# Performance work log

Hardware: AMD Instinct MI355X
Metric: run time of the kernel (lower is better)

The kernel has to match this reference:

```python
import jax, jax.numpy as jnp
import numpy as np

D, DFF, H, V, BS, NL, NG = 1024, 4096, 16, 32000, 128, 2, 2

def _ln(x, w, b, eps=1e-5):
    m = x.mean(-1, keepdims=True)
    v = ((x - m) ** 2).mean(-1, keepdims=True)
    return (x - m) / jnp.sqrt(v + eps) * w + b

def _full_attn(q, k, v):
    # q,k,v: [B,H,S,dk] ; manual max-subtract softmax with +1e-9 denom and clamp, per FullAttention
    dk = q.shape[-1]
    s = jnp.einsum('bhqd,bhkd->bhqk', q / jnp.sqrt(jnp.float32(dk)), k)
    s = s - s.max(-1, keepdims=True)
    e = jnp.exp(s)
    a = e / (e.sum(-1, keepdims=True) + 1e-9)
    a = jnp.clip(a, 1e-9, 1.0)
    return jnp.einsum('bhqk,bhkd->bhqd', a, v)

def _attn_layer(qi, ki, vi, lnw, lnb, pw, pb):
    # lnw/lnb: [4,D] (norm_q,k,v,out); pw: [4,D,D] (q,k,v,o, stored [in,out]); pb: [4,D]
    B, Sq, _ = qi.shape
    Sk = ki.shape[1]
    q = _ln(qi, lnw[0], lnb[0]) @ pw[0] + pb[0]
    k = _ln(ki, lnw[1], lnb[1]) @ pw[1] + pb[1]
    v = _ln(vi, lnw[2], lnb[2]) @ pw[2] + pb[2]
    dk = D // H
    q = q.reshape(B, Sq, H, dk).transpose(0, 2, 1, 3)
    k = k.reshape(B, Sk, H, dk).transpose(0, 2, 1, 3)
    v = v.reshape(B, Sk, H, dk).transpose(0, 2, 1, 3)
    o = _full_attn(q, k, v).transpose(0, 2, 1, 3).reshape(B, Sq, D)
    o = o @ pw[3] + pb[3]
    return _ln(o, lnw[3], lnb[3])

def _ffn(x, n1w, n1b, n2w, n2b, w1, b1, w2, b2):
    h = jax.nn.gelu(_ln(x, n1w, n1b) @ w1 + b1, approximate=False)
    return _ln(h @ w2 + b2 + x, n2w, n2b)

def _tlayer(x, lnw, lnb, pw, pb, w1, b1, w2, b2):
    # lnw/lnb: [6,D] (attn q,k,v,out norms, ffn norm1, ffn norm2)
    x = x + _attn_layer(x, x, x, lnw[:4], lnb[:4], pw, pb)
    return _ffn(x, lnw[4], lnb[4], lnw[5], lnb[5], w1, b1, w2, b2)

def _pe(S, d):
    pos = jnp.arange(S, dtype=jnp.float32)[:, None]
    div = jnp.exp(jnp.arange(0, d, 2, dtype=jnp.float32) * (-np.log(10000.0) / d))
    pe = jnp.zeros((S, d), jnp.float32)
    pe = pe.at[:, 0::2].set(jnp.sin(pos * div))
    pe = pe.at[:, 1::2].set(jnp.cos(pos * div))
    return pe

def setup_inputs() -> dict:
    key = jax.random.key(0)
    ks = iter(jax.random.split(key, 64))
    nrm = lambda shp: jax.random.normal(next(ks), shp, jnp.float32) * 0.02
    inp = {
        'x': jax.random.randint(next(ks), (4, 4096), 0, V, dtype=jnp.int32).astype(jnp.int64),
        'emb': nrm((V, D)),
        'in_ln_w': jnp.ones((D,)), 'in_ln_b': jnp.zeros((D,)),
        'loc_ln_w': jnp.ones((NL, 6, D)), 'loc_ln_b': jnp.zeros((NL, 6, D)),
        'loc_pw': nrm((NL, 4, D, D)), 'loc_pb': jnp.zeros((NL, 4, D)),
        'loc_w1': nrm((NL, D, DFF)), 'loc_b1': jnp.zeros((NL, DFF)),
        'loc_w2': nrm((NL, DFF, D)), 'loc_b2': jnp.zeros((NL, D)),
        'locn_w': jnp.ones((D,)), 'locn_b': jnp.zeros((D,)),
        'pool_q': nrm((1, 1, D)),
        'pool_n_w': jnp.ones((D,)), 'pool_n_b': jnp.zeros((D,)),
        'pool_ln_w': jnp.ones((4, D)), 'pool_ln_b': jnp.zeros((4, D)),
        'pool_pw': nrm((4, D, D)), 'pool_pb': jnp.zeros((4, D)),
        'glob_ln_w': jnp.ones((NG, 6, D)), 'glob_ln_b': jnp.zeros((NG, 6, D)),
        'glob_pw': nrm((NG, 4, D, D)), 'glob_pb': jnp.zeros((NG, 4, D)),
        'glob_w1': nrm((NG, D, DFF)), 'glob_b1': jnp.zeros((NG, DFF)),
        'glob_w2': nrm((NG, DFF, D)), 'glob_b2': jnp.zeros((NG, D)),
        'out_ln_w': jnp.ones((D,)), 'out_ln_b': jnp.zeros((D,)),
        'out_w': nrm((D, V)), 'out_b': jnp.zeros((V,)),
    }
    return inp

def reference(x, emb, in_ln_w, in_ln_b, loc_ln_w, loc_ln_b, loc_pw, loc_pb,
              loc_w1, loc_b1, loc_w2, loc_b2, locn_w, locn_b,
              pool_q, pool_n_w, pool_n_b, pool_ln_w, pool_ln_b, pool_pw, pool_pb,
              glob_ln_w, glob_ln_b, glob_pw, glob_pb, glob_w1, glob_b1, glob_w2, glob_b2,
              out_ln_w, out_ln_b, out_w, out_b):
    B, S = x.shape
    nb = S // BS
    h = jnp.clip(emb[x], -100.0, 100.0) + _pe(S, D)[None]
    h = _ln(h, in_ln_w, in_ln_b)
    h = h.reshape(B * nb, BS, D)  # local blocks
    for i in range(NL):
        h = jnp.clip(_tlayer(h, loc_ln_w[i], loc_ln_b[i], loc_pw[i], loc_pb[i],
                             loc_w1[i], loc_b1[i], loc_w2[i], loc_b2[i]), -100.0, 100.0)
    h = _ln(h, locn_w, locn_b)
    # attention pooling of each block to one vector
    hp = _ln(h, pool_n_w, pool_n_b)
    q = jnp.broadcast_to(pool_q, (B * nb, 1, D))
    g = _attn_layer(q, hp, hp, pool_ln_w, pool_ln_b, pool_pw, pool_pb)[:, 0].reshape(B, nb, D)
    for i in range(NG):
        g = jnp.clip(_tlayer(g, glob_ln_w[i], glob_ln_b[i], glob_pw[i], glob_pb[i],
                             glob_w1[i], glob_b1[i], glob_w2[i], glob_b2[i]), -100.0, 100.0)
    g = _ln(g, out_ln_w, out_ln_b)
    return g @ out_w + out_b  # [B, num_blocks, vocab]
```

## Files before the change

### kernel.cpp

```cpp
#include <hip/hip_runtime.h>
#include <hip/hip_bf16.h>
#include <math.h>

#define DEV __device__ __forceinline__

typedef __attribute__((ext_vector_type(8))) short bf16x8;
typedef __attribute__((ext_vector_type(4))) float f32x4;
typedef unsigned short u16;

constexpr int D_ = 1024, NTOK = 16384, SEQ = 4096;

DEV u16 f2b(float f){
  union{float f;unsigned u;} v; v.f=f;
  unsigned r = (v.u + 0x7fffu + ((v.u>>16)&1u))>>16;
  return (u16)r;
}
DEV float b2f(u16 h){ union{unsigned u;float f;} v; v.u=((unsigned)h)<<16; return v.f; }

DEV float gelu_f(float x){
  float z = 0.7978845608028654f*(x + 0.044715f*x*x*x);
  float e = __expf(-2.f*z);
  float t = 2.f/(1.f+e) - 1.f;
  return 0.5f*x*(1.f+t);
}

DEV void gld16(const void* g, void* l){
  __builtin_amdgcn_global_load_lds((const __attribute__((address_space(1))) void*)g,
                                   (__attribute__((address_space(3))) void*)l, 16, 0, 0);
}

DEV float blockSum(float v){
  __shared__ float sb[4];
  #pragma unroll
  for(int m=32;m>=1;m>>=1) v += __shfl_xor(v, m, 64);
  int lane = threadIdx.x & 63, wv = threadIdx.x >> 6;
  __syncthreads();
  if(lane==0) sb[wv]=v;
  __syncthreads();
  float r = sb[0]+sb[1]+sb[2]+sb[3];
  __syncthreads();
  return r;
}

__global__ __launch_bounds__(256) void detect_k(const int* __restrict__ xr, int* __restrict__ flag){
  int tid=threadIdx.x; float cnt=0.f;
  for(int i=tid;i<8192;i+=256) if(xr[2*i+1]!=0) cnt+=1.f;
  cnt = blockSum(cnt);
  if(tid==0) *flag = (cnt < 64.f) ? 1 : 0;
}

__global__ __launch_bounds__(256) void embed_k(const void* __restrict__ xv, const int* __restrict__ flag,
      const float* __restrict__ emb, const float* __restrict__ w, const float* __restrict__ b,
      u16* __restrict__ out, u16* __restrict__ outn){
  int t = blockIdx.x;
  int id;
  if(*flag) id = (int)((const long long*)xv)[t];
  else      id = ((const int*)xv)[t];
  int s = t & (SEQ-1);
  int d0 = threadIdx.x*4;
  float4 e4 = *(const float4*)(emb + (size_t)id*D_ + d0);
  float vv[4] = {e4.x, e4.y, e4.z, e4.w};
  float acc = 0.f;
  #pragma unroll
  for(int i=0;i<4;i++){
    float e = fminf(fmaxf(vv[i], -100.f), 100.f);
    int d = d0+i;
    float fr = expf(-(float)(d & ~1) * (9.210340371976184f/(float)D_));
    float ang = (float)s * fr;
    e += (d&1) ? cosf(ang) : sinf(ang);
    vv[i]=e; acc+=e;
  }
  float mean = blockSum(acc)*(1.f/D_);
  float var=0.f;
  #pragma unroll
  for(int i=0;i<4;i++){ float dd=vv[i]-mean; var+=dd*dd; }
  var = blockSum(var)*(1.f/D_);
  float rs = rsqrtf(var+1e-5f);
  float y[4];
  #pragma unroll
  for(int i=0;i<4;i++) y[i] = (vv[i]-mean)*rs*w[d0+i]+b[d0+i];
  ushort4 o; o.x=f2b(y[0]); o.y=f2b(y[1]); o.z=f2b(y[2]); o.w=f2b(y[3]);
  *(ushort4*)(out + (size_t)t*D_ + d0) = o;
  float m2 = blockSum(y[0]+y[1]+y[2]+y[3])*(1.f/D_);
  float v2=0.f;
  #pragma unroll
  for(int i=0;i<4;i++){ float dd=y[i]-m2; v2+=dd*dd; }
  v2 = blockSum(v2)*(1.f/D_);
  float rs2 = rsqrtf(v2+1e-5f);
  ushort4 on; on.x=f2b((y[0]-m2)*rs2); on.y=f2b((y[1]-m2)*rs2); on.z=f2b((y[2]-m2)*rs2); on.w=f2b((y[3]-m2)*rs2);
  *(ushort4*)(outn + (size_t)t*D_ + d0) = on;
}

template<int MODE,int WRN>
__global__ __launch_bounds__(256) void ln_k(const u16* __restrict__ in, const u16* __restrict__ res,
      const float* __restrict__ w, const float* __restrict__ b, u16* __restrict__ out,
      u16* __restrict__ outn){
  int t = blockIdx.x; int d0 = threadIdx.x*4;
  ushort4 r4 = *(const ushort4*)(in + (size_t)t*D_ + d0);
  float vv[4] = {b2f(r4.x),b2f(r4.y),b2f(r4.z),b2f(r4.w)};
  float mean = blockSum(vv[0]+vv[1]+vv[2]+vv[3])*(1.f/D_);
  float var=0.f;
  #pragma unroll
  for(int i=0;i<4;i++){ float dd=vv[i]-mean; var+=dd*dd; }
  var = blockSum(var)*(1.f/D_);
  float rs = rsqrtf(var+1e-5f);
  float rv[4]={0,0,0,0};
  if(MODE==3){
    ushort4 q4 = *(const ushort4*)(res + (size_t)t*D_ + d0);
    rv[0]=b2f(q4.x); rv[1]=b2f(q4.y); rv[2]=b2f(q4.z); rv[3]=b2f(q4.w);
  }
  float y[4];
  #pragma unroll
  for(int i=0;i<4;i++){
    float v = (vv[i]-mean)*rs;
    v = v*w[d0+i]+b[d0+i];
    if(MODE==2) v = fminf(fmaxf(v,-100.f),100.f);
    if(MODE==3) v += rv[i];
    y[i]=v;
  }
  ushort4 o; o.x=f2b(y[0]); o.y=f2b(y[1]); o.z=f2b(y[2]); o.w=f2b(y[3]);
  *(ushort4*)(out + (size_t)t*D_ + d0) = o;
  if(WRN){
    float m2 = blockSum(y[0]+y[1]+y[2]+y[3])*(1.f/D_);
    float v2=0.f;
    #pragma unroll
    for(int i=0;i<4;i++){ float dd=y[i]-m2; v2+=dd*dd; }
    v2 = blockSum(v2)*(1.f/D_);
    float rs2 = rsqrtf(v2+1e-5f);
    ushort4 on; on.x=f2b((y[0]-m2)*rs2); on.y=f2b((y[1]-m2)*rs2); on.z=f2b((y[2]-m2)*rs2); on.w=f2b((y[3]-m2)*rs2);
    *(ushort4*)(outn + (size_t)t*D_ + d0) = on;
  }
}

__global__ __launch_bounds__(256) void ln3x_k(const u16* __restrict__ in,
    const float* __restrict__ w1,const float* __restrict__ b1,
    const float* __restrict__ w2,const float* __restrict__ b2, u16* __restrict__ out){
  int t=blockIdx.x, d0=threadIdx.x*4;
  ushort4 r4 = *(const ushort4*)(in + (size_t)t*D_ + d0);
  float vv[4]={b2f(r4.x),b2f(r4.y),b2f(r4.z),b2f(r4.w)};
  #pragma unroll
  for(int pass=0;pass<3;pass++){
    float mean = blockSum(vv[0]+vv[1]+vv[2]+vv[3])*(1.f/D_);
    float var=0.f;
    #pragma unroll
    for(int i=0;i<4;i++){ float dd=vv[i]-mean; var+=dd*dd; }
    var = blockSum(var)*(1.f/D_);
    float rs = rsqrtf(var+1e-5f);
    #pragma unroll
    for(int i=0;i<4;i++){
      float y=(vv[i]-mean)*rs;
      if(pass==0) y = y*w1[d0+i]+b1[d0+i];
      else if(pass==1) y = y*w2[d0+i]+b2[d0+i];
      vv[i]=y;
    }
  }
  ushort4 o;
  o.x=f2b(vv[0]); o.y=f2b(vv[1]); o.z=f2b(vv[2]); o.w=f2b(vv[3]);
  *(ushort4*)(out + (size_t)t*D_ + d0) = o;
}

__global__ __launch_bounds__(256) void lnrow_k(const float* __restrict__ x, const float* __restrict__ w,
      const float* __restrict__ b, float* __restrict__ out){
  int d0=threadIdx.x*4;
  float vv[4]={x[d0],x[d0+1],x[d0+2],x[d0+3]};
  float mean = blockSum(vv[0]+vv[1]+vv[2]+vv[3])*(1.f/D_);
  float var=0.f;
  #pragma unroll
  for(int i=0;i<4;i++){ float dd=vv[i]-mean; var+=dd*dd; }
  var = blockSum(var)*(1.f/D_);
  float rs = rsqrtf(var+1e-5f);
  #pragma unroll
  for(int i=0;i<4;i++) out[d0+i]=(vv[i]-mean)*rs*w[d0+i]+b[d0+i];
}

__global__ __launch_bounds__(256) void tf_k(const float* __restrict__ W, int ldW,
      const float* __restrict__ lnw, u16* __restrict__ Wt, int Kd){
  __shared__ float T[64][65];
  int n0 = blockIdx.x*64, k0 = blockIdx.y*64;
  int ty = threadIdx.x>>6, tx = threadIdx.x&63;
  #pragma unroll
  for(int p=0;p<16;p++){
    int row = p*4+ty;
    float sc = lnw ? lnw[k0+row] : 1.f;
    T[row][tx] = W[(size_t)(k0+row)*ldW + n0+tx]*sc;
  }
  __syncthreads();
  #pragma unroll
  for(int p=0;p<16;p++){
    int row = p*4+ty;
    Wt[(size_t)(n0+row)*Kd + k0+tx] = f2b(T[tx][row]);
  }
}

__global__ __launch_bounds__(256) void bias_k(const float* __restrict__ W, int ldW,
      const float* __restrict__ lnb, const float* __restrict__ pb, float* __restrict__ out, int Kd){
  int j = blockIdx.x, tid=threadIdx.x;
  float chk=0.f;
  if(lnb){ for(int k=tid;k<Kd;k+=256) chk += fabsf(lnb[k]); }
  chk = blockSum(chk);
  if(chk==0.f){ if(tid==0) out[j]=pb[j]; return; }
  float s=0.f;
  for(int k=tid;k<Kd;k+=256) s += lnb[k]*W[(size_t)k*ldW + j];
  s = blockSum(s);
  if(tid==0) out[j]=pb[j]+s;
}

__global__ __launch_bounds__(256) void matvec_k(const float* __restrict__ xn, const float* __restrict__ W,
      int ldW, const float* __restrict__ bias, float* __restrict__ out){
  int j=blockIdx.x, tid=threadIdx.x;
  float s=0.f;
  for(int k=tid;k<1024;k+=256) s += xn[k]*W[(size_t)k*ldW + j];
  s=blockSum(s);
  if(tid==0) out[j]=s+bias[j];
}

template<int EPI,int OUTF,int TV>
__global__ __launch_bounds__(256) void gemm_k(const u16* __restrict__ A, const u16* __restrict__ Bt,
      const float* __restrict__ bias, const u16* __restrict__ resid, void* __restrict__ Cout,
      int M, int N, int K, int ldc){
  __shared__ u16 SH[16384];
  int tid = threadIdx.x, lane = tid&63, wv = tid>>6;
  int g = lane>>4, l15 = lane&15;
  int GX = gridDim.x;
  int nwg = GX*gridDim.y;
  int flat = blockIdx.y*GX + blockIdx.x;
  int q = nwg>>3, r = nwg&7, xcd = flat&7, idx = flat>>3;
  int f = (xcd<r ? xcd*(q+1) : r*(q+1)+(xcd-r)*q) + idx;
  int by = f/GX, bx = f - by*GX;
  int row0 = by*128, col0 = bx*128;
  int wr = wv>>1, wc = wv&1;
  u16* As = SH;
  u16* Bs = SH + 8192;
  int e0 = wv*512 + lane*8;
  f32x4 acc[4][4] = {};
  auto STAGE = [&](int buf, int k0){
    #pragma unroll
    for(int c=0;c<2;c++){
      int e = c*2048 + e0;
      gld16(A  + (size_t)(row0 + (e>>5))*K + (k0 + (e&31)), &As[buf*4096 + e]);
      gld16(Bt + (size_t)(col0 + (e>>5))*K + (k0 + (e&31)), &Bs[buf*4096 + e]);
    }
  };
  STAGE(0, 0);
  int nt = K>>5;
  __syncthreads();
  int cur = 0;
  for(int t=0;t<nt;t++){
    if(t+1<nt) STAGE(cur^1, (t+1)<<5);
    bf16x8 a[4], b[4];
    #pragma unroll
    for(int m=0;m<4;m++) a[m] = *(const bf16x8*)&As[cur*4096 + (wr*64+m*16+l15)*32 + g*8];
    #pragma unroll
    for(int n=0;n<4;n++) b[n] = *(const bf16x8*)&Bs[cur*4096 + (wc*64+n*16+l15)*32 + g*8];
    #pragma unroll
    for(int m=0;m<4;m++)
      #pragma unroll
      for(int n=0;n<4;n++)
        acc[m][n] = __builtin_amdgcn_mfma_f32_16x16x32_bf16(a[m], b[n], acc[m][n], 0,0,0);
    __syncthreads();
    cur ^= 1;
  }
  #pragma unroll
  for(int m=0;m<4;m++){
    #pragma unroll
    for(int n=0;n<4;n++){
      int Cc = col0 + wc*64 + n*16 + l15;
      float bs = bias[Cc];
      if(TV){
        int Rb = row0 + wr*64 + m*16 + g*4;
        ushort4 pk;
        pk.x = f2b(acc[m][n][0]+bs);
        pk.y = f2b(acc[m][n][1]+bs);
        pk.z = f2b(acc[m][n][2]+bs);
        pk.w = f2b(acc[m][n][3]+bs);
        *(ushort4*)((u16*)Cout + (size_t)Cc*M + Rb) = pk;
      } else {
        #pragma unroll
        for(int r2=0;r2<4;r2++){
          int R = row0 + wr*64 + m*16 + g*4 + r2;
          float v = acc[m][n][r2] + bs;
          if(EPI==1) v = gelu_f(v);
          if(EPI==2) v += b2f(resid[(size_t)R*ldc + Cc]);
          if(OUTF) ((float*)Cout)[(size_t)R*ldc + Cc] = v;
          else     ((u16*)Cout)[(size_t)R*ldc + Cc] = f2b(v);
        }
      }
    }
  }
}

__global__ __launch_bounds__(256) void attnl_k(const u16* __restrict__ QK, const u16* __restrict__ VT,
      u16* __restrict__ AT){
  __shared__ u16 SP[16384];
  __shared__ u16 Vt[8192];
  __shared__ float rmax[256], rsum[256];
  int tid=threadIdx.x, lane=tid&63, wv=tid>>6, g=lane>>4, l15=lane&15;
  int lb = blockIdx.x>>4, h = blockIdx.x&15;
  int wr=wv>>1, wc=wv&1;
  #pragma unroll
  for(int c=0;c<4;c++){
    int chunk = c*2048 + wv*512;
    int e = chunk + lane*8;
    gld16(QK + (size_t)(lb*128 + (e>>6))*2048 + h*64 + (e&63),        &SP[chunk]);
    gld16(QK + (size_t)(lb*128 + (e>>6))*2048 + 1024 + h*64 + (e&63), &SP[8192+chunk]);
    gld16(VT + (size_t)(h*64 + (e>>7))*16384 + lb*128 + (e&127),      &Vt[chunk]);
  }
  __syncthreads();
  f32x4 s[4][4] = {};
  #pragma unroll
  for(int ks=0;ks<2;ks++){
    bf16x8 a[4], b[4];
    #pragma unroll
    for(int m=0;m<4;m++) a[m] = *(const bf16x8*)&SP[(wr*64+m*16+l15)*64 + ks*32 + g*8];
    #pragma unroll
    for(int n=0;n<4;n++) b[n] = *(const bf16x8*)&SP[8192+(wc*64+n*16+l15)*64 + ks*32 + g*8];
    #pragma unroll
    for(int m=0;m<4;m++)
      #pragma unroll
      for(int n=0;n<4;n++)
        s[m][n] = __builtin_amdgcn_mfma_f32_16x16x32_bf16(a[m], b[n], s[m][n], 0,0,0);
  }
  #pragma unroll
  for(int m=0;m<4;m++)
    #pragma unroll
    for(int n=0;n<4;n++) s[m][n] *= 0.125f;
  #pragma unroll
  for(int m=0;m<4;m++)
    #pragma unroll
    for(int r=0;r<4;r++){
      float mx = fmaxf(fmaxf(s[m][0][r],s[m][1][r]),fmaxf(s[m][2][r],s[m][3][r]));
      #pragma unroll
      for(int msk=1;msk<16;msk<<=1) mx = fmaxf(mx, __shfl_xor(mx,msk,64));
      if(l15==0) rmax[(wr*64+m*16+g*4+r)*2+wc]=mx;
    }
  __syncthreads();
  #pragma unroll
  for(int m=0;m<4;m++)
    #pragma unroll
    for(int r=0;r<4;r++){
      int row = wr*64+m*16+g*4+r;
      float M2 = fmaxf(rmax[row*2], rmax[row*2+1]);
      float sm=0.f;
      #pragma unroll
      for(int n=0;n<4;n++){ float e = expf(s[m][n][r]-M2); s[m][n][r]=e; sm+=e; }
      #pragma unroll
      for(int msk=1;msk<16;msk<<=1) sm += __shfl_xor(sm,msk,64);
      if(l15==0) rsum[row*2+wc]=sm;
    }
  __syncthreads();
  #pragma unroll
  for(int m=0;m<4;m++)
    #pragma unroll
    for(int r=0;r<4;r++){
      int row = wr*64+m*16+g*4+r;
      float den = rsum[row*2]+rsum[row*2+1]+1e-9f;
      #pragma unroll
      for(int n=0;n<4;n++){
        float a = s[m][n][r]/den;
        a = fminf(fmaxf(a,1e-9f),1.f);
        SP[row*128 + wc*64+n*16+l15] = f2b(a);
      }
    }
  __syncthreads();
  f32x4 o[4][2] = {};
  #pragma unroll
  for(int ks=0;ks<4;ks++){
    bf16x8 a[4], b[2];
    #pragma unroll
    for(int m=0;m<4;m++) a[m] = *(const bf16x8*)&SP[(wr*64+m*16+l15)*128 + ks*32 + g*8];
    #pragma unroll
    for(int n=0;n<2;n++) b[n] = *(const bf16x8*)&Vt[(wc*32+n*16+l15)*128 + ks*32 + g*8];
    #pragma unroll
    for(int m=0;m<4;m++)
      #pragma unroll
      for(int n=0;n<2;n++)
        o[m][n] = __builtin_amdgcn_mfma_f32_16x16x32_bf16(a[m], b[n], o[m][n], 0,0,0);
  }
  #pragma unroll
  for(int m=0;m<4;m++)
    #pragma unroll
    for(int n=0;n<2;n++)
      #pragma unroll
      for(int r=0;r<4;r++)
        AT[(size_t)(lb*128 + wr*64+m*16+g*4+r)*1024 + h*64 + wc*32+n*16+l15] = f2b(o[m][n][r]);
}

__global__ __launch_bounds__(256) void poolattn_k(const float* __restrict__ qp, const u16* __restrict__ KV,
      u16* __restrict__ g0){
  int lb = blockIdx.x, tid = threadIdx.x;
  __shared__ float sc[16*128];
  for(int p=tid;p<2048;p+=256){
    int h=p>>7, j=p&127;
    const u16* krow = KV + (size_t)(lb*128+j)*2048 + h*64;
    float s=0.f;
    for(int d=0;d<64;d++) s += qp[h*64+d]*b2f(krow[d]);
    sc[h*128+j] = s*0.125f;
  }
  __syncthreads();
  if(tid<16){
    float* r=&sc[tid*128];
    float mx=r[0];
    for(int j=1;j<128;j++) mx=fmaxf(mx,r[j]);
    float sm=0.f;
    for(int j=0;j<128;j++){ float e=expf(r[j]-mx); r[j]=e; sm+=e; }
    sm+=1e-9f;
    for(int j=0;j<128;j++) r[j]=fminf(fmaxf(r[j]/sm,1e-9f),1.f);
  }
  __syncthreads();
  for(int c=tid;c<1024;c+=256){
    int h=c>>6;
    float acc=0.f;
    for(int j=0;j<128;j++) acc += sc[h*128+j]*b2f(KV[(size_t)(lb*128+j)*2048 + 1024 + c]);
    g0[(size_t)lb*1024 + c] = f2b(acc);
  }
}

__global__ __launch_bounds__(256) void attng_k(const u16* __restrict__ QKV, u16* __restrict__ OUT){
  int bb = blockIdx.x>>4, h = blockIdx.x&15;
  __shared__ float sc[32*32];
  int tid=threadIdx.x;
  for(int p=tid;p<1024;p+=256){
    int i=p>>5, j=p&31;
    const u16* q = QKV + (size_t)(bb*32+i)*3072 + h*64;
    const u16* k = QKV + (size_t)(bb*32+j)*3072 + 1024 + h*64;
    float s=0.f;
    for(int d=0;d<64;d++) s += b2f(q[d])*b2f(k[d]);
    sc[p] = s*0.125f;
  }
  __syncthreads();
  if(tid<32){
    float* r=&sc[tid*32];
    float mx=r[0];
    for(int j=1;j<32;j++) mx=fmaxf(mx,r[j]);
    float sm=0.f;
    for(int j=0;j<32;j++){ float e=expf(r[j]-mx); r[j]=e; sm+=e; }
    sm+=1e-9f;
    for(int j=0;j<32;j++) r[j]=fminf(fmaxf(r[j]/sm,1e-9f),1.f);
  }
  __syncthreads();
  for(int p=tid;p<2048;p+=256){
    int i=p>>6, d=p&63;
    float acc=0.f;
    for(int j=0;j<32;j++) acc += sc[i*32+j]*b2f(QKV[(size_t)(bb*32+j)*3072 + 2048 + h*64 + d]);
    OUT[(size_t)(bb*32+i)*1024 + h*64 + d] = f2b(acc);
  }
}

extern "C" void kernel_launch(void* const* d_in, const int* in_sizes, int n_in,
                              void* d_out, int out_size, void* d_ws, size_t ws_size,
                              hipStream_t stream) {
  (void)in_sizes; (void)n_in; (void)out_size;
  const void*  x       = d_in[0];
  const float* emb     = (const float*)d_in[1];
  const float* in_ln_w = (const float*)d_in[2];
  const float* in_ln_b = (const float*)d_in[3];
  const float* loc_ln_w= (const float*)d_in[4];
  const float* loc_ln_b= (const float*)d_in[5];
  const float* loc_pw  = (const float*)d_in[6];
  const float* loc_pb  = (const float*)d_in[7];
  const float* loc_w1  = (const float*)d_in[8];
  const float* loc_b1  = (const float*)d_in[9];
  const float* loc_w2  = (const float*)d_in[10];
  const float* loc_b2  = (const float*)d_in[11];
  const float* locn_w  = (const float*)d_in[12];
  const float* locn_b  = (const float*)d_in[13];
  const float* pool_q  = (const float*)d_in[14];
  const float* pool_n_w= (const float*)d_in[15];
  const float* pool_n_b= (const float*)d_in[16];
  const float* pool_ln_w=(const float*)d_in[17];
  const float* pool_ln_b=(const float*)d_in[18];
  const float* pool_pw = (const float*)d_in[19];
  const float* pool_pb = (const float*)d_in[20];
  const float* glob_ln_w=(const float*)d_in[21];
  const float* glob_ln_b=(const float*)d_in[22];
  const float* glob_pw = (const float*)d_in[23];
  const float* glob_pb = (const float*)d_in[24];
  const float* glob_w1 = (const float*)d_in[25];
  const float* glob_b1 = (const float*)d_in[26];
  const float* glob_w2 = (const float*)d_in[27];
  const float* glob_b2 = (const float*)d_in[28];
  const float* out_ln_w= (const float*)d_in[29];
  const float* out_ln_b= (const float*)d_in[30];
  const float* out_w   = (const float*)d_in[31];
  const float* out_b   = (const float*)d_in[32];

  char* wsb = (char*)d_ws;
  size_t off = 0;
  auto AL = [&](size_t n)->char*{ size_t o=(off+255)&~(size_t)255; off=o+n; return wsb+o; };

  int*  flag = (int*)AL(256);
  u16*  WA   = (u16*)AL(12ull*1024*1024*2);
  float* BA  = (float*)AL(12*1024*4);
  float* qn  = (float*)AL(1024*4);
  float* qp  = (float*)AL(1024*4);
  float* Hb  = (float*)AL(32000*4);
  u16*  R    = (u16*)AL(64ull*1024*1024*2);
  u16*  X    = (u16*)AL((size_t)NTOK*1024*2);
  u16*  XN   = (u16*)AL((size_t)NTOK*1024*2);
  u16*  G    = (u16*)AL(128ull*1024*2);
  u16*  GN   = (u16*)AL(128ull*1024*2);
  u16*  GQKV = (u16*)AL(128ull*3072*2);
  u16*  GAT  = (u16*)AL(128ull*1024*2);
  u16*  GO   = (u16*)AL(128ull*1024*2);
  u16*  GFH  = (u16*)AL(128ull*4096*2);
  u16*  g0   = (u16*)AL(128ull*1024*2);
  if(off > ws_size) return;

  u16 *LWqk = WA, *LWv = WA+2097152, *LWo = WA+3145728, *LW1 = WA+4194304, *LW2 = WA+8388608;
  float *Lbqk = BA, *Lbv = BA+2048, *Lbo = BA+3072, *Lb1 = BA+4096, *Lb2 = BA+8192;
  u16 *GWqkv = WA, *GWo = WA+3145728, *GW1 = WA+4194304, *GW2 = WA+8388608;
  float *Gbqkv = BA, *Gbo = BA+3072, *Gb1 = BA+4096, *Gb2 = BA+8192;
  u16 *PWkv = WA, *PWo = WA+2097152;
  float *Pbkv = BA, *Pbo = BA+2048;
  u16 *QKb = R, *VTb = R+33554432, *ATb = R+50331648;
  u16 *FH  = R;
  u16 *KVb = R;
  u16 *HW  = R;
  u16 *Ob  = XN;

  const size_t MM = 1024ull*1024;

  detect_k<<<1,256,0,stream>>>((const int*)x, flag);
  embed_k<<<NTOK,256,0,stream>>>(x, flag, emb, in_ln_w, in_ln_b, X, XN);

  for(int l=0;l<2;l++){
    const float* pw = loc_pw + (size_t)l*4*MM;
    const float* lw = loc_ln_w + (size_t)l*6*1024;
    const float* lb = loc_ln_b + (size_t)l*6*1024;
    const float* pb = loc_pb + (size_t)l*4*1024;
    tf_k<<<dim3(16,16),256,0,stream>>>(pw+0*MM, 1024, lw+0*1024, LWqk,          1024);
    tf_k<<<dim3(16,16),256,0,stream>>>(pw+1*MM, 1024, lw+1*1024, LWqk+1024*1024,1024);
    tf_k<<<dim3(16,16),256,0,stream>>>(pw+2*MM, 1024, lw+2*1024, LWv,           1024);
    tf_k<<<dim3(16,16),256,0,stream>>>(pw+3*MM, 1024, nullptr,   LWo,           1024);
    tf_k<<<dim3(64,16),256,0,stream>>>(loc_w1+(size_t)l*1024*4096, 4096, lw+4*1024, LW1, 1024);
    tf_k<<<dim3(16,64),256,0,stream>>>(loc_w2+(size_t)l*4096*1024, 1024, nullptr,   LW2, 4096);
    bias_k<<<1024,256,0,stream>>>(pw+0*MM, 1024, lb+0*1024, pb+0,      Lbqk,      1024);
    bias_k<<<1024,256,0,stream>>>(pw+1*MM, 1024, lb+1*1024, pb+1024,   Lbqk+1024, 1024);
    bias_k<<<1024,256,0,stream>>>(pw+2*MM, 1024, lb+2*1024, pb+2*1024, Lbv,       1024);
    bias_k<<<1024,256,0,stream>>>(pw+3*MM, 1024, nullptr,   pb+3*1024, Lbo,       1024);
    bias_k<<<4096,256,0,stream>>>(loc_w1+(size_t)l*1024*4096, 4096, lb+4*1024, loc_b1+(size_t)l*4096, Lb1, 1024);
    bias_k<<<1024,256,0,stream>>>(loc_w2+(size_t)l*4096*1024, 1024, nullptr,   loc_b2+(size_t)l*1024, Lb2, 4096);

    gemm_k<0,0,0><<<dim3(16,128),256,0,stream>>>(XN, LWqk, Lbqk, nullptr, QKb, NTOK, 2048, 1024, 2048);
    gemm_k<0,0,1><<<dim3(8,128),256,0,stream>>>(XN, LWv, Lbv, nullptr, VTb, NTOK, 1024, 1024, 0);
    attnl_k<<<128*16,256,0,stream>>>(QKb, VTb, ATb);
    gemm_k<0,0,0><<<dim3(8,128),256,0,stream>>>(ATb, LWo, Lbo, nullptr, Ob, NTOK, 1024, 1024, 1024);
    ln_k<3,1><<<NTOK,256,0,stream>>>(Ob, X, lw+3*1024, lb+3*1024, X, XN);
    gemm_k<1,0,0><<<dim3(32,128),256,0,stream>>>(XN, LW1, Lb1, nullptr, FH, NTOK, 4096, 1024, 4096);
    gemm_k<2,0,0><<<dim3(8,128),256,0,stream>>>(FH, LW2, Lb2, X, Ob, NTOK, 1024, 4096, 1024);
    ln_k<2,1><<<NTOK,256,0,stream>>>(Ob, nullptr, lw+5*1024, lb+5*1024, X, XN);
  }

  tf_k<<<dim3(16,16),256,0,stream>>>(pool_pw+1*MM, 1024, pool_ln_w+1024,   PWkv,           1024);
  tf_k<<<dim3(16,16),256,0,stream>>>(pool_pw+2*MM, 1024, pool_ln_w+2*1024, PWkv+1024*1024, 1024);
  tf_k<<<dim3(16,16),256,0,stream>>>(pool_pw+3*MM, 1024, nullptr,          PWo,            1024);
  bias_k<<<1024,256,0,stream>>>(pool_pw+1*MM, 1024, pool_ln_b+1024,   pool_pb+1024,   Pbkv,      1024);
  bias_k<<<1024,256,0,stream>>>(pool_pw+2*MM, 1024, pool_ln_b+2*1024, pool_pb+2*1024, Pbkv+1024, 1024);
  bias_k<<<1024,256,0,stream>>>(pool_pw+3*MM, 1024, nullptr,          pool_pb+3*1024, Pbo,       1024);
  lnrow_k<<<1,256,0,stream>>>(pool_q, pool_ln_w, pool_ln_b, qn);
  matvec_k<<<1024,256,0,stream>>>(qn, pool_pw, 1024, pool_pb, qp);
  ln3x_k<<<NTOK,256,0,stream>>>(X, locn_w, locn_b, pool_n_w, pool_n_b, XN);
  gemm_k<0,0,0><<<dim3(16,128),256,0,stream>>>(XN, PWkv, Pbkv, nullptr, KVb, NTOK, 2048, 1024, 2048);
  poolattn_k<<<128,256,0,stream>>>(qp, KVb, g0);
  gemm_k<0,0,0><<<dim3(8,1),256,0,stream>>>(g0, PWo, Pbo, nullptr, GO, 128, 1024, 1024, 1024);
  ln_k<1,1><<<128,256,0,stream>>>(GO, nullptr, pool_ln_w+3*1024, pool_ln_b+3*1024, G, GN);

  for(int l=0;l<2;l++){
    const float* pw = glob_pw + (size_t)l*4*MM;
    const float* lw = glob_ln_w + (size_t)l*6*1024;
    const float* lb = glob_ln_b + (size_t)l*6*1024;
    const float* pb = glob_pb + (size_t)l*4*1024;
    tf_k<<<dim3(16,16),256,0,stream>>>(pw+0*MM, 1024, lw+0*1024, GWqkv,            1024);
    tf_k<<<dim3(16,16),256,0,stream>>>(pw+1*MM, 1024, lw+1*1024, GWqkv+1024*1024,  1024);
    tf_k<<<dim3(16,16),256,0,stream>>>(pw+2*MM, 1024, lw+2*1024, GWqkv+2048*1024,  1024);
    tf_k<<<dim3(16,16),256,0,stream>>>(pw+3*MM, 1024, nullptr,   GWo,              1024);
    tf_k<<<dim3(64,16),256,0,stream>>>(glob_w1+(size_t)l*1024*4096, 4096, lw+4*1024, GW1, 1024);
    tf_k<<<dim3(16,64),256,0,stream>>>(glob_w2+(size_t)l*4096*1024, 1024, nullptr,   GW2, 4096);
    bias_k<<<1024,256,0,stream>>>(pw+0*MM, 1024, lb+0*1024, pb+0,      Gbqkv,      1024);
    bias_k<<<1024,256,0,stream>>>(pw+1*MM, 1024, lb+1*1024, pb+1024,   Gbqkv+1024, 1024);
    bias_k<<<1024,256,0,stream>>>(pw+2*MM, 1024, lb+2*1024, pb+2*1024, Gbqkv+2048, 1024);
    bias_k<<<1024,256,0,stream>>>(pw+3*MM, 1024, nullptr,   pb+3*1024, Gbo,        1024);
    bias_k<<<4096,256,0,stream>>>(glob_w1+(size_t)l*1024*4096, 4096, lb+4*1024, glob_b1+(size_t)l*4096, Gb1, 1024);
    bias_k<<<1024,256,0,stream>>>(glob_w2+(size_t)l*4096*1024, 1024, nullptr,   glob_b2+(size_t)l*1024, Gb2, 4096);

    gemm_k<0,0,0><<<dim3(24,1),256,0,stream>>>(GN, GWqkv, Gbqkv, nullptr, GQKV, 128, 3072, 1024, 3072);
    attng_k<<<64,256,0,stream>>>(GQKV, GAT);
    gemm_k<0,0,0><<<dim3(8,1),256,0,stream>>>(GAT, GWo, Gbo, nullptr, GO, 128, 1024, 1024, 1024);
    ln_k<3,1><<<128,256,0,stream>>>(GO, G, lw+3*1024, lb+3*1024, G, GN);
    gemm_k<1,0,0><<<dim3(32,1),256,0,stream>>>(GN, GW1, Gb1, nullptr, GFH, 128, 4096, 1024, 4096);
    gemm_k<2,0,0><<<dim3(8,1),256,0,stream>>>(GFH, GW2, Gb2, G, GO, 128, 1024, 4096, 1024);
    ln_k<2,1><<<128,256,0,stream>>>(GO, nullptr, lw+5*1024, lb+5*1024, G, GN);
  }

  tf_k<<<dim3(500,16),256,0,stream>>>(out_w, 32000, out_ln_w, HW, 1024);
  bias_k<<<32000,256,0,stream>>>(out_w, 32000, out_ln_b, out_b, Hb, 1024);
  gemm_k<0,1,0><<<dim3(250,1),256,0,stream>>>(GN, HW, Hb, nullptr, d_out, 128, 32000, 1024, 32000);
}
```

Baseline: 2.365 ms.

## Add 256x256-tile ping-pong bf16 GEMM kernel for large local-layer projections

Introduces gemm256_k, a 512-thread GEMM with 256x256 output tiles and 128KB of dynamic LDS double buffers. It loads directly from global memory into swizzled LDS, remaps workgroups so they are spread across XCDs, and interleaves staging loads with MFMA quarters using explicit waitcnts, barriers and setprio. All large token-dimension GEMMs in the local layers and the pooling K/V projection switch to it. The goal is more data reuse per tile and better overlap of memory with MFMA work. In exchange it depends on a large dynamic LDS allocation with no function attribute set, hand-tuned vmcnt counts, and dimensions that must divide by 256.

After: 2.800 ms. 18.4% more time.

```diff
diff --git a/kernel.cpp b/kernel.cpp
--- a/kernel.cpp
+++ b/kernel.cpp
@@ -28,6 +28,11 @@
   __builtin_amdgcn_global_load_lds((const __attribute__((address_space(1))) void*)g,
                                    (__attribute__((address_space(3))) void*)l, 16, 0, 0);
 }
+
+#define BAR()   __builtin_amdgcn_s_barrier()
+#define LGKM0() asm volatile("s_waitcnt lgkmcnt(0)" ::: "memory")
+#define VM6()   asm volatile("s_waitcnt vmcnt(6)" ::: "memory")
+#define VM0()   asm volatile("s_waitcnt vmcnt(0)" ::: "memory")
 
 DEV float blockSum(float v){
   __shared__ float sb[4];
@@ -283,6 +288,135 @@
           if(EPI==2) v += b2f(resid[(size_t)R*ldc + Cc]);
           if(OUTF) ((float*)Cout)[(size_t)R*ldc + Cc] = v;
           else     ((u16*)Cout)[(size_t)R*ldc + Cc] = f2b(v);
+        }
+      }
+    }
+  }
+}
+
+template<int EPI,int TV>
+__global__ __launch_bounds__(512,2) void gemm256_k(const u16* __restrict__ A, const u16* __restrict__ Bt,
+      const float* __restrict__ bias, const u16* __restrict__ resid, void* __restrict__ Cout,
+      int M, int N, int K, int ldc){
+  extern __shared__ char smem[];
+  u16* LS = (u16*)smem;
+  int tid = threadIdx.x, lane = tid&63, wid = tid>>6;
+  int g = lane>>4, l15 = lane&15;
+  int wm = wid>>2, wn = wid&3;
+  int GX = gridDim.x, nwg = GX*gridDim.y;
+  int flat = blockIdx.y*GX + blockIdx.x;
+  int q = nwg>>3, r = nwg&7, xcd = flat&7, idx = flat>>3;
+  int f = (xcd<r ? xcd*(q+1) : r*(q+1)+(xcd-r)*q) + idx;
+  int by = f/GX, bx = f - by*GX;
+  int row0 = by*256, col0 = bx*256;
+  int NT = K>>6, NI = NT>>1;
+  int srcsw = (((lane&7)^(lane>>3))<<3);
+  int rdsw  = ((l15&7)<<3);
+
+  f32x4 acc[8][4] = {};
+  bf16x8 afr[2][4], bfr[2][4];
+
+  auto STAGE_A = [&](int b, int H, int t){
+    #pragma unroll
+    for(int j=0;j<2;j++){
+      int c = j*8 + wid;
+      int grow = row0 + H*128 + c*8 + (lane>>3);
+      gld16(A + (size_t)grow*K + t*64 + srcsw, smem + b*32768 + H*16384 + c*1024);
+    }
+  };
+  auto STAGE_B = [&](int b, int H, int t){
+    #pragma unroll
+    for(int j=0;j<2;j++){
+      int c = j*8 + wid;
+      int grow = col0 + H*128 + c*8 + (lane>>3);
+      gld16(Bt + (size_t)grow*K + t*64 + srcsw, smem + 65536 + b*32768 + H*16384 + c*1024);
+    }
+  };
+  auto READ_A = [&](int b, int mh){
+    #pragma unroll
+    for(int ks=0;ks<2;ks++)
+      #pragma unroll
+      for(int m=0;m<4;m++)
+        afr[ks][m] = *(const bf16x8*)&LS[b*16384 + wm*8192 + (mh*64+m*16+l15)*64 + ((ks*32+g*8)^rdsw)];
+  };
+  auto READ_B = [&](int b){
+    #pragma unroll
+    for(int ks=0;ks<2;ks++)
+      #pragma unroll
+      for(int n=0;n<4;n++)
+        bfr[ks][n] = *(const bf16x8*)&LS[32768 + b*16384 + (wn>>1)*8192 + (((wn&1)*64+n*16+l15)*64) + ((ks*32+g*8)^rdsw)];
+  };
+  auto MFMA_Q = [&](int mh, int nh){
+    __builtin_amdgcn_s_setprio(1);
+    #pragma unroll
+    for(int ks=0;ks<2;ks++)
+      #pragma unroll
+      for(int m=0;m<4;m++)
+        #pragma unroll
+        for(int n=0;n<2;n++)
+          acc[mh*4+m][nh*2+n] = __builtin_amdgcn_mfma_f32_16x16x32_bf16(
+              afr[ks][m], bfr[ks][nh*2+n], acc[mh*4+m][nh*2+n], 0,0,0);
+    __builtin_amdgcn_s_setprio(0);
+  };
+
+  STAGE_A(0,0,0); STAGE_A(0,1,0); STAGE_B(0,0,0); STAGE_B(0,1,0);
+  STAGE_B(1,0,1); STAGE_B(1,1,1); STAGE_A(1,0,1);
+  VM6();
+  BAR();
+
+  for(int i=0;i<NI;i++){
+    int t0 = 2*i, t1 = 2*i+1;
+    bool lastI = (i==NI-1);
+    READ_B(0); READ_A(0,0);
+    STAGE_A(1,1,t1);
+    LGKM0();
+    BAR(); MFMA_Q(0,0); BAR();
+    if(t0+2<NT) STAGE_B(0,0,t0+2);
+    BAR(); MFMA_Q(0,1); BAR();
+    READ_A(0,1);
+    if(t0+2<NT) STAGE_B(0,1,t0+2);
+    LGKM0();
+    BAR(); MFMA_Q(1,0); BAR();
+    if(t0+2<NT) STAGE_A(0,0,t0+2);
+    if(lastI){ VM0(); } else { VM6(); }
+    BAR(); MFMA_Q(1,1); BAR();
+    READ_B(1); READ_A(1,0);
+    if(t0+2<NT) STAGE_A(0,1,t0+2);
+    LGKM0();
+    BAR(); MFMA_Q(0,0); BAR();
+    if(t1+2<NT) STAGE_B(1,0,t1+2);
+    BAR(); MFMA_Q(0,1); BAR();
+    READ_A(1,1);
+    if(t1+2<NT) STAGE_B(1,1,t1+2);
+    LGKM0();
+    BAR(); MFMA_Q(1,0); BAR();
+    if(t1+2<NT) STAGE_A(1,0,t1+2);
+    VM6();
+    BAR(); MFMA_Q(1,1); BAR();
+  }
+
+  #pragma unroll
+  for(int mi=0;mi<8;mi++){
+    #pragma unroll
+    for(int n=0;n<4;n++){
+      int Cc = col0 + wn*64 + n*16 + l15;
+      float bs = bias[Cc];
+      if(TV){
+        int Rb = row0 + wm*128 + mi*16 + g*4;
+        ushort4 pk;
+        pk.x = f2b(acc[mi][n][0]+bs);
+        pk.y = f2b(acc[mi][n][1]+bs);
+        pk.z = f2b(acc[mi][n][2]+bs);
+        pk.w = f2b(acc[mi][n][3]+bs);
+        *(ushort4*)((u16*)Cout + (size_t)Cc*M + Rb) = pk;
+      } else {
+        #pragma unroll
+        for(int r2=0;r2<4;r2++){
+          int R = row0 + wm*128 + mi*16 + g*4 + r2;
+          float v = acc[mi][n][r2] + bs;
+          if(EPI==1) v = gelu_f(v);
+          if(EPI==2) v += b2f(resid[(size_t)R*ldc + Cc]);
+          ((u16*)Cout)[(size_t)R*ldc + Cc] = f2b(v);
         }
       }
     }
@@ -519,6 +653,7 @@
   u16 *Ob  = XN;
 
   const size_t MM = 1024ull*1024;
+  const size_t SM256 = 131072;
 
   detect_k<<<1,256,0,stream>>>((const int*)x, flag);
   embed_k<<<NTOK,256,0,stream>>>(x, flag, emb, in_ln_w, in_ln_b, X, XN);
@@ -541,13 +676,13 @@
     bias_k<<<4096,256,0,stream>>>(loc_w1+(size_t)l*1024*4096, 4096, lb+4*1024, loc_b1+(size_t)l*4096, Lb1, 1024);
     bias_k<<<1024,256,0,stream>>>(loc_w2+(size_t)l*4096*1024, 1024, nullptr,   loc_b2+(size_t)l*1024, Lb2, 4096);
 
-    gemm_k<0,0,0><<<dim3(16,128),256,0,stream>>>(XN, LWqk, Lbqk, nullptr, QKb, NTOK, 2048, 1024, 2048);
-    gemm_k<0,0,1><<<dim3(8,128),256,0,stream>>>(XN, LWv, Lbv, nullptr, VTb, NTOK, 1024, 1024, 0);
+    gemm256_k<0,0><<<dim3(8,64),512,SM256,stream>>>(XN, LWqk, Lbqk, nullptr, QKb, NTOK, 2048, 1024, 2048);
+    gemm256_k<0,1><<<dim3(4,64),512,SM256,stream>>>(XN, LWv, Lbv, nullptr, VTb, NTOK, 1024, 1024, 0);
     attnl_k<<<128*16,256,0,stream>>>(QKb, VTb, ATb);
-    gemm_k<0,0,0><<<dim3(8,128),256,0,stream>>>(ATb, LWo, Lbo, nullptr, Ob, NTOK, 1024, 1024, 1024);
+    gemm256_k<0,0><<<dim3(4,64),512,SM256,stream>>>(ATb, LWo, Lbo, nullptr, Ob, NTOK, 1024, 1024, 1024);
     ln_k<3,1><<<NTOK,256,0,stream>>>(Ob, X, lw+3*1024, lb+3*1024, X, XN);
-    gemm_k<1,0,0><<<dim3(32,128),256,0,stream>>>(XN, LW1, Lb1, nullptr, FH, NTOK, 4096, 1024, 4096);
-    gemm_k<2,0,0><<<dim3(8,128),256,0,stream>>>(FH, LW2, Lb2, X, Ob, NTOK, 1024, 4096, 1024);
+    gemm256_k<1,0><<<dim3(16,64),512,SM256,stream>>>(XN, LW1, Lb1, nullptr, FH, NTOK, 4096, 1024, 4096);
+    gemm256_k<2,0><<<dim3(4,64),512,SM256,stream>>>(FH, LW2, Lb2, X, Ob, NTOK, 1024, 4096, 1024);
     ln_k<2,1><<<NTOK,256,0,stream>>>(Ob, nullptr, lw+5*1024, lb+5*1024, X, XN);
   }
 
@@ -560,7 +695,7 @@
   lnrow_k<<<1,256,0,stream>>>(pool_q, pool_ln_w, pool_ln_b, qn);
   matvec_k<<<1024,256,0,stream>>>(qn, pool_pw, 1024, pool_pb, qp);
   ln3x_k<<<NTOK,256,0,stream>>>(X, locn_w, locn_b, pool_n_w, pool_n_b, XN);
-  gemm_k<0,0,0><<<dim3(16,128),256,0,stream>>>(XN, PWkv, Pbkv, nullptr, KVb, NTOK, 2048, 1024, 2048);
+  gemm256_k<0,0><<<dim3(8,64),512,SM256,stream>>>(XN, PWkv, Pbkv, nullptr, KVb, NTOK, 2048, 1024, 2048);
   poolattn_k<<<128,256,0,stream>>>(qp, KVb, g0);
   gemm_k<0,0,0><<<dim3(8,1),256,0,stream>>>(g0, PWo, Pbo, nullptr, GO, 128, 1024, 1024, 1024);
   ln_k<1,1><<<128,256,0,stream>>>(GO, nullptr, pool_ln_w+3*1024, pool_ln_b+3*1024, G, GN);
```

## Batch weight-prep launches into fused kernels and coalesce transposed GEMM output via LDS

Applied to the files above, without the earlier changes.

Replaces the many per-matrix weight transpose and bias-fold launches in each layer and in the pooling stage with single multi-matrix kernels that dispatch on block index. This cuts launch count and lets small grids run together. Separately, the transposed-output GEMM epilogue now stages results in swizzled shared memory and writes contiguous ushort4 rows instead of scattered 4-element stores. That adds a barrier and LDS traffic to the epilogue.

Result: faster. 2.158 ms (-8.8%).

```diff
diff --git a/kernel.cpp b/kernel.cpp
--- a/kernel.cpp
+++ b/kernel.cpp
@@ -173,36 +173,111 @@
   for(int i=0;i<4;i++) out[d0+i]=(vv[i]-mean)*rs*w[d0+i]+b[d0+i];
 }
 
+#define TF_BODY(W, ldW, lnw, Wt, Kd, n0, k0)                                 \
+  {                                                                          \
+    int ty = threadIdx.x>>6, tx = threadIdx.x&63;                            \
+    _Pragma("unroll")                                                        \
+    for(int p=0;p<16;p++){                                                   \
+      int row = p*4+ty;                                                      \
+      float sc = (lnw) ? (lnw)[(k0)+row] : 1.f;                              \
+      T[row][tx] = (W)[(size_t)((k0)+row)*(ldW) + (n0)+tx]*sc;               \
+    }                                                                        \
+    __syncthreads();                                                         \
+    _Pragma("unroll")                                                        \
+    for(int p=0;p<16;p++){                                                   \
+      int row = p*4+ty;                                                      \
+      (Wt)[(size_t)((n0)+row)*(Kd) + (k0)+tx] = f2b(T[tx][row]);             \
+    }                                                                        \
+  }
+
 __global__ __launch_bounds__(256) void tf_k(const float* __restrict__ W, int ldW,
       const float* __restrict__ lnw, u16* __restrict__ Wt, int Kd){
   __shared__ float T[64][65];
   int n0 = blockIdx.x*64, k0 = blockIdx.y*64;
-  int ty = threadIdx.x>>6, tx = threadIdx.x&63;
-  #pragma unroll
-  for(int p=0;p<16;p++){
-    int row = p*4+ty;
-    float sc = lnw ? lnw[k0+row] : 1.f;
-    T[row][tx] = W[(size_t)(k0+row)*ldW + n0+tx]*sc;
-  }
-  __syncthreads();
-  #pragma unroll
-  for(int p=0;p<16;p++){
-    int row = p*4+ty;
-    Wt[(size_t)(n0+row)*Kd + k0+tx] = f2b(T[tx][row]);
-  }
+  TF_BODY(W, ldW, lnw, Wt, Kd, n0, k0)
+}
+
+__global__ __launch_bounds__(256) void prep_tf_layer_k(const float* __restrict__ pw,
+      const float* __restrict__ w1, const float* __restrict__ w2, const float* __restrict__ lw,
+      u16* __restrict__ Wqk, u16* __restrict__ Wv, u16* __restrict__ Wo,
+      u16* __restrict__ W1t, u16* __restrict__ W2t){
+  __shared__ float T[64][65];
+  int bid = blockIdx.x;
+  const float* W; int ldW; const float* lnw; u16* Wt; int Kd, n0, k0;
+  if(bid < 1024){
+    int m = bid>>8, t = bid&255;
+    n0 = (t&15)*64; k0 = (t>>4)*64;
+    W = pw + (size_t)m*1024*1024; ldW = 1024; Kd = 1024;
+    lnw = (m<3) ? lw + m*1024 : nullptr;
+    Wt = (m==0)?Wqk : (m==1)?(Wqk+1024*1024) : (m==2)?Wv : Wo;
+  } else if(bid < 2048){
+    int t = bid-1024;
+    n0 = (t&63)*64; k0 = (t>>6)*64;
+    W = w1; ldW = 4096; Kd = 1024; lnw = lw+4*1024; Wt = W1t;
+  } else {
+    int t = bid-2048;
+    n0 = (t&15)*64; k0 = (t>>4)*64;
+    W = w2; ldW = 1024; Kd = 4096; lnw = nullptr; Wt = W2t;
+  }
+  TF_BODY(W, ldW, lnw, Wt, Kd, n0, k0)
+}
+
+__global__ __launch_bounds__(256) void prep_tf_pool_k(const float* __restrict__ pw,
+      const float* __restrict__ lw, u16* __restrict__ PWkv, u16* __restrict__ PWo){
+  __shared__ float T[64][65];
+  int bid = blockIdx.x;
+  int m = 1 + (bid>>8), t = bid&255;
+  int n0 = (t&15)*64, k0 = (t>>4)*64;
+  const float* W = pw + (size_t)m*1024*1024;
+  const float* lnw = (m<3) ? lw + m*1024 : nullptr;
+  u16* Wt = (m==1)?PWkv : (m==2)?(PWkv+1024*1024) : PWo;
+  TF_BODY(W, 1024, lnw, Wt, 1024, n0, k0)
+}
+
+DEV void bias_body(const float* W, int ldW, int Kd, const float* lnb, float pbv, float* out){
+  int tid = threadIdx.x;
+  float chk = 0.f;
+  if(lnb){ for(int k=tid;k<Kd;k+=256) chk += fabsf(lnb[k]); }
+  chk = blockSum(chk);
+  if(chk==0.f){ if(tid==0) *out = pbv; return; }
+  float s=0.f;
+  for(int k=tid;k<Kd;k+=256) s += lnb[k]*W[(size_t)k*ldW];
+  s = blockSum(s);
+  if(tid==0) *out = pbv + s;
 }
 
 __global__ __launch_bounds__(256) void bias_k(const float* __restrict__ W, int ldW,
       const float* __restrict__ lnb, const float* __restrict__ pb, float* __restrict__ out, int Kd){
-  int j = blockIdx.x, tid=threadIdx.x;
-  float chk=0.f;
-  if(lnb){ for(int k=tid;k<Kd;k+=256) chk += fabsf(lnb[k]); }
-  chk = blockSum(chk);
-  if(chk==0.f){ if(tid==0) out[j]=pb[j]; return; }
-  float s=0.f;
-  for(int k=tid;k<Kd;k+=256) s += lnb[k]*W[(size_t)k*ldW + j];
-  s = blockSum(s);
-  if(tid==0) out[j]=pb[j]+s;
+  int j = blockIdx.x;
+  bias_body(W + j, ldW, Kd, lnb, pb[j], out + j);
+}
+
+__global__ __launch_bounds__(256) void prep_bias_layer_k(const float* __restrict__ pw,
+      const float* __restrict__ w1, const float* __restrict__ w2,
+      const float* __restrict__ lb, const float* __restrict__ pb,
+      const float* __restrict__ b1in, const float* __restrict__ b2in,
+      float* __restrict__ Bqk, float* __restrict__ Bv, float* __restrict__ Bo,
+      float* __restrict__ B1, float* __restrict__ B2){
+  int j = blockIdx.x;
+  const float* W; int ldW, Kd; const float* lnb; float pbv; float* out;
+  const size_t MM = 1024ull*1024;
+  if(j<2048){ int m=j>>10; int col=j&1023; W=pw+m*MM+col; ldW=1024; Kd=1024; lnb=lb+m*1024; pbv=pb[m*1024+col]; out=Bqk+j; }
+  else if(j<3072){ int col=j-2048; W=pw+2*MM+col; ldW=1024; Kd=1024; lnb=lb+2*1024; pbv=pb[2*1024+col]; out=Bv+col; }
+  else if(j<4096){ int col=j-3072; W=pw+3*MM+col; ldW=1024; Kd=1024; lnb=nullptr; pbv=pb[3*1024+col]; out=Bo+col; }
+  else if(j<8192){ int col=j-4096; W=w1+col; ldW=4096; Kd=1024; lnb=lb+4*1024; pbv=b1in[col]; out=B1+col; }
+  else { int col=j-8192; W=w2+col; ldW=1024; Kd=4096; lnb=nullptr; pbv=b2in[col]; out=B2+col; }
+  bias_body(W, ldW, Kd, lnb, pbv, out);
+}
+
+__global__ __launch_bounds__(256) void prep_bias_pool_k(const float* __restrict__ pw,
+      const float* __restrict__ lb, const float* __restrict__ pb,
+      float* __restrict__ Pbkv, float* __restrict__ Pbo){
+  int j = blockIdx.x;
+  const size_t MM = 1024ull*1024;
+  int m = 1 + (j>>10), col = j&1023;
+  const float* lnb = (m<3) ? lb + m*1024 : nullptr;
+  float* out = (m==1)?(Pbkv+col) : (m==2)?(Pbkv+1024+col) : (Pbo+col);
+  bias_body(pw + m*MM + col, 1024, 1024, lnb, pb[m*1024+col], out);
 }
 
 __global__ __launch_bounds__(256) void matvec_k(const float* __restrict__ xn, const float* __restrict__ W,
@@ -260,21 +335,36 @@
     __syncthreads();
     cur ^= 1;
   }
-  #pragma unroll
-  for(int m=0;m<4;m++){
-    #pragma unroll
-    for(int n=0;n<4;n++){
-      int Cc = col0 + wc*64 + n*16 + l15;
-      float bs = bias[Cc];
-      if(TV){
-        int Rb = row0 + wr*64 + m*16 + g*4;
-        ushort4 pk;
-        pk.x = f2b(acc[m][n][0]+bs);
-        pk.y = f2b(acc[m][n][1]+bs);
-        pk.z = f2b(acc[m][n][2]+bs);
-        pk.w = f2b(acc[m][n][3]+bs);
-        *(ushort4*)((u16*)Cout + (size_t)Cc*M + Rb) = pk;
-      } else {
+  if(TV){
+    u16* Tb = SH;
+    #pragma unroll
+    for(int m=0;m<4;m++){
+      #pragma unroll
+      for(int n=0;n<4;n++){
+        int c = wc*64 + n*16 + l15;
+        float bs = bias[col0 + c];
+        #pragma unroll
+        for(int r2=0;r2<4;r2++){
+          int Rl = wr*64 + m*16 + g*4 + r2;
+          Tb[c*128 + (Rl ^ ((c&7)<<4))] = f2b(acc[m][n][r2]+bs);
+        }
+      }
+    }
+    __syncthreads();
+    for(int p=tid*4; p<16384; p+=1024){
+      int c = p>>7, rr = p&127;
+      int rs = rr ^ ((c&7)<<4);
+      ushort4 v4;
+      v4.x = Tb[c*128+rs]; v4.y = Tb[c*128+rs+1]; v4.z = Tb[c*128+rs+2]; v4.w = Tb[c*128+rs+3];
+      *(ushort4*)((u16*)Cout + (size_t)(col0+c)*M + row0 + rr) = v4;
+    }
+  } else {
+    #pragma unroll
+    for(int m=0;m<4;m++){
+      #pragma unroll
+      for(int n=0;n<4;n++){
+        int Cc = col0 + wc*64 + n*16 + l15;
+        float bs = bias[Cc];
         #pragma unroll
         for(int r2=0;r2<4;r2++){
           int R = row0 + wr*64 + m*16 + g*4 + r2;
@@ -528,18 +618,11 @@
     const float* lw = loc_ln_w + (size_t)l*6*1024;
     const float* lb = loc_ln_b + (size_t)l*6*1024;
     const float* pb = loc_pb + (size_t)l*4*1024;
-    tf_k<<<dim3(16,16),256,0,stream>>>(pw+0*MM, 1024, lw+0*1024, LWqk,          1024);
-    tf_k<<<dim3(16,16),256,0,stream>>>(pw+1*MM, 1024, lw+1*1024, LWqk+1024*1024,1024);
-    tf_k<<<dim3(16,16),256,0,stream>>>(pw+2*MM, 1024, lw+2*1024, LWv,           1024);
-    tf_k<<<dim3(16,16),256,0,stream>>>(pw+3*MM, 1024, nullptr,   LWo,           1024);
-    tf_k<<<dim3(64,16),256,0,stream>>>(loc_w1+(size_t)l*1024*4096, 4096, lw+4*1024, LW1, 1024);
-    tf_k<<<dim3(16,64),256,0,stream>>>(loc_w2+(size_t)l*4096*1024, 1024, nullptr,   LW2, 4096);
-    bias_k<<<1024,256,0,stream>>>(pw+0*MM, 1024, lb+0*1024, pb+0,      Lbqk,      1024);
-    bias_k<<<1024,256,0,stream>>>(pw+1*MM, 1024, lb+1*1024, pb+1024,   Lbqk+1024, 1024);
-    bias_k<<<1024,256,0,stream>>>(pw+2*MM, 1024, lb+2*1024, pb+2*1024, Lbv,       1024);
-    bias_k<<<1024,256,0,stream>>>(pw+3*MM, 1024, nullptr,   pb+3*1024, Lbo,       1024);
-    bias_k<<<4096,256,0,stream>>>(loc_w1+(size_t)l*1024*4096, 4096, lb+4*1024, loc_b1+(size_t)l*4096, Lb1, 1024);
-    bias_k<<<1024,256,0,stream>>>(loc_w2+(size_t)l*4096*1024, 1024, nullptr,   loc_b2+(size_t)l*1024, Lb2, 4096);
+    const float* w1 = loc_w1 + (size_t)l*1024*4096;
+    const float* w2 = loc_w2 + (size_t)l*4096*1024;
+    prep_tf_layer_k<<<3072,256,0,stream>>>(pw, w1, w2, lw, LWqk, LWv, LWo, LW1, LW2);
+    prep_bias_layer_k<<<9216,256,0,stream>>>(pw, w1, w2, lb, pb,
+        loc_b1+(size_t)l*4096, loc_b2+(size_t)l*1024, Lbqk, Lbv, Lbo, Lb1, Lb2);
 
     gemm_k<0,0,0><<<dim3(16,128),256,0,stream>>>(XN, LWqk, Lbqk, nullptr, QKb, NTOK, 2048, 1024, 2048);
     gemm_k<0,0,1><<<dim3(8,128),256,0,stream>>>(XN, LWv, Lbv, nullptr, VTb, NTOK, 1024, 1024, 0);
@@ -551,12 +634,8 @@
     ln_k<2,1><<<NTOK,256,0,stream>>>(Ob, nullptr, lw+5*1024, lb+5*1024, X, XN);
   }
 
-  tf_k<<<dim3(16,16),256,0,stream>>>(pool_pw+1*MM, 1024, pool_ln_w+1024,   PWkv,           1024);
-  tf_k<<<dim3(16,16),256,0,stream>>>(pool_pw+2*MM, 1024, pool_ln_w+2*1024, PWkv+1024*1024, 1024);
-  tf_k<<<dim3(16,16),256,0,stream>>>(pool_pw+3*MM, 1024, nullptr,          PWo,            1024);
-  bias_k<<<1024,256,0,stream>>>(pool_pw+1*MM, 1024, pool_ln_b+1024,   pool_pb+1024,   Pbkv,      1024);
-  bias_k<<<1024,256,0,stream>>>(pool_pw+2*MM, 1024, pool_ln_b+2*1024, pool_pb+2*1024, Pbkv+1024, 1024);
-  bias_k<<<1024,256,0,stream>>>(pool_pw+3*MM, 1024, nullptr,          pool_pb+3*1024, Pbo,       1024);
+  prep_tf_pool_k<<<768,256,0,stream>>>(pool_pw, pool_ln_w, PWkv, PWo);
+  prep_bias_pool_k<<<3072,256,0,stream>>>(pool_pw, pool_ln_b, pool_pb, Pbkv, Pbo);
   lnrow_k<<<1,256,0,stream>>>(pool_q, pool_ln_w, pool_ln_b, qn);
   matvec_k<<<1024,256,0,stream>>>(qn, pool_pw, 1024, pool_pb, qp);
   ln3x_k<<<NTOK,256,0,stream>>>(X, locn_w, locn_b, pool_n_w, pool_n_b, XN);
@@ -570,18 +649,11 @@
     const float* lw = glob_ln_w + (size_t)l*6*1024;
     const float* lb = glob_ln_b + (size_t)l*6*1024;
     const float* pb = glob_pb + (size_t)l*4*1024;
-    tf_k<<<dim3(16,16),256,0,stream>>>(pw+0*MM, 1024, lw+0*1024, GWqkv,            1024);
-    tf_k<<<dim3(16,16),256,0,stream>>>(pw+1*MM, 1024, lw+1*1024, GWqkv+1024*1024,  1024);
-    tf_k<<<dim3(16,16),256,0,stream>>>(pw+2*MM, 1024, lw+2*1024, GWqkv+2048*1024,  1024);
-    tf_k<<<dim3(16,16),256,0,stream>>>(pw+3*MM, 1024, nullptr,   GWo,              1024);
-    tf_k<<<dim3(64,16),256,0,stream>>>(glob_w1+(size_t)l*1024*4096, 4096, lw+4*1024, GW1, 1024);
-    tf_k<<<dim3(16,64),256,0,stream>>>(glob_w2+(size_t)l*4096*1024, 1024, nullptr,   GW2, 4096);
-    bias_k<<<1024,256,0,stream>>>(pw+0*MM, 1024, lb+0*1024, pb+0,      Gbqkv,      1024);
-    bias_k<<<1024,256,0,stream>>>(pw+1*MM, 1024, lb+1*1024, pb+1024,   Gbqkv+1024, 1024);
-    bias_k<<<1024,256,0,stream>>>(pw+2*MM, 1024, lb+2*1024, pb+2*1024, Gbqkv+2048, 1024);
-    bias_k<<<1024,256,0,stream>>>(pw+3*MM, 1024, nullptr,   pb+3*1024, Gbo,        1024);
-    bias_k<<<4096,256,0,stream>>>(glob_w1+(size_t)l*1024*4096, 4096, lb+4*1024, glob_b1+(size_t)l*4096, Gb1, 1024);
-    bias_k<<<1024,256,0,stream>>>(glob_w2+(size_t)l*4096*1024, 1024, nullptr,   glob_b2+(size_t)l*1024, Gb2, 4096);
+    const float* w1 = glob_w1 + (size_t)l*1024*4096;
+    const float* w2 = glob_w2 + (size_t)l*4096*1024;
+    prep_tf_layer_k<<<3072,256,0,stream>>>(pw, w1, w2, lw, GWqkv, GWqkv+2097152, GWo, GW1, GW2);
+    prep_bias_layer_k<<<9216,256,0,stream>>>(pw, w1, w2, lb, pb,
+        glob_b1+(size_t)l*4096, glob_b2+(size_t)l*1024, Gbqkv, Gbqkv+2048, Gbo, Gb1, Gb2);
 
     gemm_k<0,0,0><<<dim3(24,1),256,0,stream>>>(GN, GWqkv, Gbqkv, nullptr, GQKV, 128, 3072, 1024, 3072);
     attng_k<<<64,256,0,stream>>>(GQKV, GAT);
```
